# Optimization experiments

Measured on AMD Instinct MI355X. Metric: run time of the kernel, lower is better.

## Reference

```python
import jax, jax.numpy as jnp
import numpy as np

NUM_USERS = 100000
NUM_ITEMS = 50000
D = 64            # args.recdim
N_LAYERS = 3      # args.layer
NNZ = 4800000     # edges in the normalized bipartite adjacency (COO)
N = NUM_USERS + NUM_ITEMS


def setup_inputs() -> dict:
    key = jax.random.key(0)
    k1, k2, k3, k4, k5 = jax.random.split(key, 5)
    # LightGCN inits embeddings with normal(std=0.1)
    user_emb = 0.1 * jax.random.normal(k1, (NUM_USERS, D), dtype=jnp.float32)
    item_emb = 0.1 * jax.random.normal(k2, (NUM_ITEMS, D), dtype=jnp.float32)
    adj_rows = jax.random.randint(k3, (NNZ,), 0, N)
    adj_cols = jax.random.randint(k4, (NNZ,), 0, N)
    # stand-in for D^{-1/2} A D^{-1/2} normalized values
    adj_vals = jax.random.uniform(k5, (NNZ,), dtype=jnp.float32)
    return {"user_emb": user_emb, "item_emb": item_emb,
            "adj_vals": adj_vals, "adj_rows": adj_rows, "adj_cols": adj_cols}


def _spmm(rows, cols, vals, x, n):
    # sparse [n,n] @ dense [n,d] via gather + segment-sum (COO SpMM)
    return jax.ops.segment_sum(vals[:, None] * x[cols], rows, num_segments=n)


def reference(user_emb, item_emb, adj_vals, adj_rows, adj_cols):
    n_users = user_emb.shape[0]
    n = n_users + item_emb.shape[0]
    all_emb = jnp.concatenate([user_emb, item_emb], axis=0)  # [N, D]
    embs = [all_emb]
    for _ in range(N_LAYERS):  # fixed small hop count
        all_emb = _spmm(adj_rows, adj_cols, adj_vals, all_emb, n)
        embs.append(all_emb)
    light_out = jnp.mean(jnp.stack(embs, axis=1), axis=1)  # [N, D]
    users = light_out[:n_users]
    items = light_out[n_users:]
    return users, items
```

## Files before the change

### kernel.cpp

```cpp
#include <hip/hip_runtime.h>


#define NUSERS 100000
#define NITEMS 50000
#define NTOT   150000
#define DIM    64
#define NNZ_E  4800000

#define RPB     256
#define RSH     8
#define NBUCK   586
#define CHUNK_E 16384
#define NPART   ((NNZ_E + CHUNK_E - 1) / CHUNK_E)
#define NBIN    (64 * 37)
#define NOCT    (NBUCK * 64)

__device__ __forceinline__ unsigned short benc(float f) {
    union { float f; unsigned u; } t; t.f = f;
    unsigned r = t.u + 0x7FFFu + ((t.u >> 16) & 1u);
    return (unsigned short)(r >> 16);
}
__device__ __forceinline__ float blo(unsigned g) { return __uint_as_float(g << 16); }
__device__ __forceinline__ float bhi(unsigned g) { return __uint_as_float(g & 0xFFFF0000u); }

__global__ void __launch_bounds__(1024)
partA1_kernel(const int* __restrict__ rows, int* __restrict__ cntmatT) {
    __shared__ int l[NBUCK];
    int p = blockIdx.x;
    int c0 = p * CHUNK_E;
    int c1 = c0 + CHUNK_E; if (c1 > NNZ_E) c1 = NNZ_E;
    for (int k = threadIdx.x; k < NBUCK; k += 1024) l[k] = 0;
    __syncthreads();
    for (int e = c0 + threadIdx.x; e < c1; e += 1024)
        atomicAdd(&l[rows[e] >> RSH], 1);
    __syncthreads();
    for (int k = threadIdx.x; k < NBUCK; k += 1024)
        cntmatT[(size_t)k * NPART + p] = l[k];
}

__global__ void __launch_bounds__(512)
colscan1_kernel(const int* __restrict__ cntmatT, int* __restrict__ runoffT,
                int* __restrict__ colTotal) {
    __shared__ int t[512];
    int b = blockIdx.x;
    int tid = threadIdx.x;
    int v = (tid < NPART) ? cntmatT[(size_t)b * NPART + tid] : 0;
    t[tid] = v;
    __syncthreads();
    for (int ofs = 1; ofs < 512; ofs <<= 1) {
        int a = (tid >= ofs) ? t[tid - ofs] : 0;
        __syncthreads();
        t[tid] += a;
        __syncthreads();
    }
    if (tid < NPART) runoffT[(size_t)b * NPART + tid] = t[tid] - v;
    if (tid == NPART - 1) colTotal[b] = t[tid];
}

__global__ void __launch_bounds__(1024)
colscan2_kernel(const int* __restrict__ colTotal, int* __restrict__ bptr) {
    __shared__ int t[1024];
    int tid = threadIdx.x;
    int v = (tid < NBUCK) ? colTotal[tid] : 0;
    t[tid] = v;
    __syncthreads();
    for (int ofs = 1; ofs < 1024; ofs <<= 1) {
        int a = (tid >= ofs) ? t[tid - ofs] : 0;
        __syncthreads();
        t[tid] += a;
        __syncthreads();
    }
    if (tid < NBUCK) bptr[tid] = t[tid] - v;
    if (tid == 1023) bptr[NBUCK] = t[1023];
}

__global__ void __launch_bounds__(1024)
partA2_kernel(const int* __restrict__ rows, const int* __restrict__ cols,
              const float* __restrict__ vals, const int* __restrict__ runoffT,
              const int* __restrict__ bptr, int2* __restrict__ tmp) {
    __shared__ int cur[NBUCK];
    int p = blockIdx.x;
    int c0 = p * CHUNK_E;
    int c1 = c0 + CHUNK_E; if (c1 > NNZ_E) c1 = NNZ_E;
    for (int k = threadIdx.x; k < NBUCK; k += 1024)
        cur[k] = bptr[k] + runoffT[(size_t)k * NPART + p];
    __syncthreads();
    for (int e = c0 + threadIdx.x; e < c1; e += 1024) {
        int r = rows[e];
        int b = r >> RSH, rl = r & (RPB - 1);
        int q = atomicAdd(&cur[b], 1);
        tmp[q] = make_int2(cols[e] | (rl << 18), __float_as_int(vals[e]));
    }
}

__global__ void __launch_bounds__(1024)
partBF_kernel(const int* __restrict__ bptr, const int2* __restrict__ tmp,
              unsigned* __restrict__ fin, int* __restrict__ optr) {
    __shared__ int cnt[NBIN];
    __shared__ int base[NBIN];
    __shared__ int st[1024];
    int b = blockIdx.x;
    int bb0 = bptr[b];
    int nb = bptr[b + 1] - bb0;
    int tid = threadIdx.x;
    for (int k = tid; k < NBIN; k += 1024) cnt[k] = 0;
    __syncthreads();
    for (int k = tid; k < nb; k += 1024) {
        int x = tmp[bb0 + k].x;
        int key = ((x >> 20) & 63) * 37 + ((x & 0x3FFFF) >> 12);
        atomicAdd(&cnt[key], 1);
    }
    __syncthreads();
    int t0 = tid * 3;
    int c0 = (t0     < NBIN) ? cnt[t0]     : 0;
    int c1 = (t0 + 1 < NBIN) ? cnt[t0 + 1] : 0;
    int c2 = (t0 + 2 < NBIN) ? cnt[t0 + 2] : 0;
    int s = c0 + c1 + c2;
    st[tid] = s;
    __syncthreads();
    for (int ofs = 1; ofs < 1024; ofs <<= 1) {
        int a = (tid >= ofs) ? st[tid - ofs] : 0;
        __syncthreads();
        st[tid] += a;
        __syncthreads();
    }
    int P = st[tid] - s;
    if (t0     < NBIN) base[t0]     = P;
    if (t0 + 1 < NBIN) base[t0 + 1] = P + c0;
    if (t0 + 2 < NBIN) base[t0 + 2] = P + c0 + c1;
    __syncthreads();
    if (tid < 64) optr[b * 64 + tid] = bb0 + base[tid * 37];
    if (b == NBUCK - 1 && tid == 0) optr[NBUCK * 64] = bb0 + nb;
    __syncthreads();
    for (int k = tid; k < nb; k += 1024) {
        int2 t = tmp[bb0 + k];
        int x = t.x;
        int key = ((x >> 20) & 63) * 37 + ((x & 0x3FFFF) >> 12);
        int q = atomicAdd(&base[key], 1);
        unsigned qq = (unsigned)__float2int_rn(__int_as_float(t.y) * 4096.f);
        if (qq > 4095u) qq = 4095u;
        fin[bb0 + q] = ((unsigned)x & 0xFFFFFu) | (qq << 20);
    }
}

__global__ void convert_kernel(const float2* __restrict__ user, const float2* __restrict__ item,
                               unsigned* __restrict__ xh2) {
    int i = blockIdx.x * blockDim.x + threadIdx.x;
    if (i >= NTOT * 32) return;
    float2 v = (i < NUSERS * 32) ? user[i] : item[i - NUSERS * 32];
    xh2[i] = (unsigned)benc(v.x) | ((unsigned)benc(v.y) << 16);
}

__global__ void __launch_bounds__(256)
spmm4_kernel(const int* __restrict__ optr, const unsigned* __restrict__ ed,
             const uint4* __restrict__ xin, uint4* __restrict__ yout,
             const float4* __restrict__ user, const float4* __restrict__ item,
             const uint4* __restrict__ y1, float4* __restrict__ out, int last) {
    int wid  = blockIdx.x * 4 + (threadIdx.x >> 6);
    int lane = threadIdx.x & 63;
    int g    = wid * 8 + (lane >> 3);
    int s    = lane & 7;
    int i    = optr[g];
    int end  = optr[g + 1];
    const float SCL = 1.f / 4096.f;
    float4 A00 = {0,0,0,0}, A01 = {0,0,0,0};
    float4 A10 = {0,0,0,0}, A11 = {0,0,0,0};
    float4 A20 = {0,0,0,0}, A21 = {0,0,0,0};
    float4 A30 = {0,0,0,0}, A31 = {0,0,0,0};

#define PROC(E, G) do { \
        float v  = (float)((E) >> 20) * SCL; \
        int   k  = ((E) >> 18) & 3; \
        float s0 = (k == 0) ? v : 0.f, s1 = (k == 1) ? v : 0.f; \
        float s2 = (k == 2) ? v : 0.f, s3 = (k == 3) ? v : 0.f; \
        float f0 = blo((G).x), f1 = bhi((G).x), f2 = blo((G).y), f3 = bhi((G).y); \
        float f4_ = blo((G).z), f5 = bhi((G).z), f6 = blo((G).w), f7 = bhi((G).w); \
        A00.x += s0*f0; A00.y += s0*f1; A00.z += s0*f2; A00.w += s0*f3; \
        A01.x += s0*f4_; A01.y += s0*f5; A01.z += s0*f6; A01.w += s0*f7; \
        A10.x += s1*f0; A10.y += s1*f1; A10.z += s1*f2; A10.w += s1*f3; \
        A11.x += s1*f4_; A11.y += s1*f5; A11.z += s1*f6; A11.w += s1*f7; \
        A20.x += s2*f0; A20.y += s2*f1; A20.z += s2*f2; A20.w += s2*f3; \
        A21.x += s2*f4_; A21.y += s2*f5; A21.z += s2*f6; A21.w += s2*f7; \
        A30.x += s3*f0; A30.y += s3*f1; A30.z += s3*f2; A30.w += s3*f3; \
        A31.x += s3*f4_; A31.y += s3*f5; A31.z += s3*f6; A31.w += s3*f7; \
    } while (0)

    for (; i + 4 <= end; i += 4) {
        unsigned e0 = ed[i], e1 = ed[i + 1], e2 = ed[i + 2], e3 = ed[i + 3];
        uint4 g0 = xin[(size_t)(e0 & 0x3FFFF) * 8 + s];
        uint4 g1 = xin[(size_t)(e1 & 0x3FFFF) * 8 + s];
        uint4 g2 = xin[(size_t)(e2 & 0x3FFFF) * 8 + s];
        uint4 g3 = xin[(size_t)(e3 & 0x3FFFF) * 8 + s];
        PROC(e0, g0); PROC(e1, g1); PROC(e2, g2); PROC(e3, g3);
    }
    for (; i < end; ++i) {
        unsigned e = ed[i];
        uint4 gg = xin[(size_t)(e & 0x3FFFF) * 8 + s];
        PROC(e, gg);
    }
#undef PROC

    if (!last) {
#define EPI(K, AK0, AK1) do { \
        int r = g * 4 + (K); \
        if (r < NTOT) { \
            uint4 o; \
            o.x = (unsigned)benc(AK0.x) | ((unsigned)benc(AK0.y) << 16); \
            o.y = (unsigned)benc(AK0.z) | ((unsigned)benc(AK0.w) << 16); \
            o.z = (unsigned)benc(AK1.x) | ((unsigned)benc(AK1.y) << 16); \
            o.w = (unsigned)benc(AK1.z) | ((unsigned)benc(AK1.w) << 16); \
            yout[(size_t)r * 8 + s] = o; \
        } \
    } while (0)
        EPI(0, A00, A01); EPI(1, A10, A11); EPI(2, A20, A21); EPI(3, A30, A31);
#undef EPI
    } else {
#define EPI(K, AK0, AK1) do { \
        int r = g * 4 + (K); \
        if (r < NTOT) { \
            size_t f4 = (size_t)r * 16 + 2 * s; \
            float4 x0a = (r < NUSERS) ? user[f4]     : item[f4     - (size_t)NUSERS * 16]; \
            float4 x0b = (r < NUSERS) ? user[f4 + 1] : item[f4 + 1 - (size_t)NUSERS * 16]; \
            uint4 u1 = y1[(size_t)r * 8 + s]; \
            uint4 u2 = xin[(size_t)r * 8 + s]; \
            float4 oa, ob; \
            oa.x = 0.25f * (x0a.x + blo(u1.x) + blo(u2.x) + AK0.x); \
            oa.y = 0.25f * (x0a.y + bhi(u1.x) + bhi(u2.x) + AK0.y); \
            oa.z = 0.25f * (x0a.z + blo(u1.y) + blo(u2.y) + AK0.z); \
            oa.w = 0.25f * (x0a.w + bhi(u1.y) + bhi(u2.y) + AK0.w); \
            ob.x = 0.25f * (x0b.x + blo(u1.z) + blo(u2.z) + AK1.x); \
            ob.y = 0.25f * (x0b.y + bhi(u1.z) + bhi(u2.z) + AK1.y); \
            ob.z = 0.25f * (x0b.z + blo(u1.w) + blo(u2.w) + AK1.z); \
            ob.w = 0.25f * (x0b.w + bhi(u1.w) + bhi(u2.w) + AK1.w); \
            out[f4]     = oa; \
            out[f4 + 1] = ob; \
        } \
    } while (0)
        EPI(0, A00, A01); EPI(1, A10, A11); EPI(2, A20, A21); EPI(3, A30, A31);
#undef EPI
    }
}

extern "C" void kernel_launch(void* const* d_in, const int* in_sizes, int n_in,
                              void* d_out, int out_size, void* d_ws, size_t ws_size,
                              hipStream_t stream) {
    const float* user = (const float*)d_in[0];
    const float* item = (const float*)d_in[1];
    const float* vals = (const float*)d_in[2];
    const int*   rows = (const int*)d_in[3];
    const int*   cols = (const int*)d_in[4];
    float* out = (float*)d_out;

    char* w = (char*)d_ws;
    int2*     tmp      = (int2*)w;     w += (size_t)NNZ_E * 8;
    unsigned* fin      = (unsigned*)w; w += (size_t)NNZ_E * 4;
    unsigned* bufA     = (unsigned*)w; w += (size_t)NTOT * DIM * 2;
    unsigned* bufB     = (unsigned*)w; w += (size_t)NTOT * DIM * 2;
    int*      cntmatT  = (int*)w;      w += (size_t)NBUCK * NPART * 4;
    int*      runoffT  = (int*)w;      w += (size_t)NBUCK * NPART * 4;
    int*      optr     = (int*)w;      w += (size_t)(NOCT + 1) * 4;
    int*      colTotal = (int*)w;      w += (size_t)NBUCK * 4;
    int*      bptr     = (int*)w;

    const int blk = 256;
    const int gConv = (NTOT * 32 + blk - 1) / blk;
    const int gSpmm = NOCT / 32;

    partA1_kernel<<<NPART, 1024, 0, stream>>>(rows, cntmatT);
    colscan1_kernel<<<NBUCK, 512, 0, stream>>>(cntmatT, runoffT, colTotal);
    colscan2_kernel<<<1, 1024, 0, stream>>>(colTotal, bptr);
    partA2_kernel<<<NPART, 1024, 0, stream>>>(rows, cols, vals, runoffT, bptr, tmp);
    partBF_kernel<<<NBUCK, 1024, 0, stream>>>(bptr, tmp, fin, optr);

    convert_kernel<<<gConv, blk, 0, stream>>>((const float2*)user, (const float2*)item, bufA);

    spmm4_kernel<<<gSpmm, blk, 0, stream>>>(optr, fin, (const uint4*)bufA, (uint4*)bufB,
                                            (const float4*)user, (const float4*)item,
                                            (const uint4*)bufB, (float4*)out, 0);
    spmm4_kernel<<<gSpmm, blk, 0, stream>>>(optr, fin, (const uint4*)bufB, (uint4*)bufA,
                                            (const float4*)user, (const float4*)item,
                                            (const uint4*)bufB, (float4*)out, 0);
    spmm4_kernel<<<gSpmm, blk, 0, stream>>>(optr, fin, (const uint4*)bufA, (uint4*)bufA,
                                            (const float4*)user, (const float4*)item,
                                            (const uint4*)bufB, (float4*)out, 1);
}
```

Baseline: 492.2 us.

## Sort edges locally in shared memory per chunk and gather segments in bucket pass

The first partition pass now sorts each chunk's edges by bucket in LDS and writes the chunk out contiguously, instead of scattering each edge straight to its global bucket position. The bucket pass then locates each bucket's segments across chunks with a binary search over per-chunk offsets. The chunk size is halved to fit the LDS buffer, and the fine-bin count is doubled with a smaller column shift, which changes the edge ordering inside each octet. The aim is to replace scattered global writes with coalesced ones, at the cost of scattered-segment reads and a binary search per edge in the bucket pass.

```diff
diff --git a/kernel.cpp b/kernel.cpp
--- a/kernel.cpp
+++ b/kernel.cpp
@@ -10,9 +10,11 @@
 #define RPB     256
 #define RSH     8
 #define NBUCK   586
-#define CHUNK_E 16384
+#define CHUNK_E 8192
 #define NPART   ((NNZ_E + CHUNK_E - 1) / CHUNK_E)
-#define NBIN    (64 * 37)
+#define NCB     74
+#define CSH     11
+#define NBIN    (64 * NCB)
 #define NOCT    (NBUCK * 64)
 
 __device__ __forceinline__ unsigned short benc(float f) {
@@ -23,38 +25,41 @@
 __device__ __forceinline__ float blo(unsigned g) { return __uint_as_float(g << 16); }
 __device__ __forceinline__ float bhi(unsigned g) { return __uint_as_float(g & 0xFFFF0000u); }
 
-__global__ void __launch_bounds__(1024)
-partA1_kernel(const int* __restrict__ rows, int* __restrict__ cntmatT) {
+__global__ void __launch_bounds__(512)
+partA1_kernel(const int* __restrict__ rows, int* __restrict__ cntmat) {
     __shared__ int l[NBUCK];
     int p = blockIdx.x;
     int c0 = p * CHUNK_E;
     int c1 = c0 + CHUNK_E; if (c1 > NNZ_E) c1 = NNZ_E;
-    for (int k = threadIdx.x; k < NBUCK; k += 1024) l[k] = 0;
-    __syncthreads();
-    for (int e = c0 + threadIdx.x; e < c1; e += 1024)
+    for (int k = threadIdx.x; k < NBUCK; k += 512) l[k] = 0;
+    __syncthreads();
+    for (int e = c0 + threadIdx.x; e < c1; e += 512)
         atomicAdd(&l[rows[e] >> RSH], 1);
     __syncthreads();
-    for (int k = threadIdx.x; k < NBUCK; k += 1024)
-        cntmatT[(size_t)k * NPART + p] = l[k];
-}
-
-__global__ void __launch_bounds__(512)
-colscan1_kernel(const int* __restrict__ cntmatT, int* __restrict__ runoffT,
+    for (int k = threadIdx.x; k < NBUCK; k += 512)
+        cntmat[(size_t)p * NBUCK + k] = l[k];
+}
+
+__global__ void __launch_bounds__(1024)
+colscan1_kernel(const int* __restrict__ cntmat, int* __restrict__ runoffT,
                 int* __restrict__ colTotal) {
-    __shared__ int t[512];
+    __shared__ int t[1024];
     int b = blockIdx.x;
     int tid = threadIdx.x;
-    int v = (tid < NPART) ? cntmatT[(size_t)b * NPART + tid] : 0;
+    int v = (tid < NPART) ? cntmat[(size_t)tid * NBUCK + b] : 0;
     t[tid] = v;
     __syncthreads();
-    for (int ofs = 1; ofs < 512; ofs <<= 1) {
+    for (int ofs = 1; ofs < 1024; ofs <<= 1) {
         int a = (tid >= ofs) ? t[tid - ofs] : 0;
         __syncthreads();
         t[tid] += a;
         __syncthreads();
     }
-    if (tid < NPART) runoffT[(size_t)b * NPART + tid] = t[tid] - v;
-    if (tid == NPART - 1) colTotal[b] = t[tid];
+    if (tid < NPART) runoffT[(size_t)b * (NPART + 1) + tid] = t[tid] - v;
+    if (tid == NPART - 1) {
+        runoffT[(size_t)b * (NPART + 1) + NPART] = t[tid];
+        colTotal[b] = t[tid];
+    }
 }
 
 __global__ void __launch_bounds__(1024)
@@ -74,48 +79,78 @@
     if (tid == 1023) bptr[NBUCK] = t[1023];
 }
 
-__global__ void __launch_bounds__(1024)
+__global__ void __launch_bounds__(512)
 partA2_kernel(const int* __restrict__ rows, const int* __restrict__ cols,
-              const float* __restrict__ vals, const int* __restrict__ runoffT,
-              const int* __restrict__ bptr, int2* __restrict__ tmp) {
+              const float* __restrict__ vals, const int* __restrict__ cntmat,
+              int* __restrict__ segoff, int2* __restrict__ tmp) {
+    __shared__ int2 buf[CHUNK_E];
     __shared__ int cur[NBUCK];
+    __shared__ int st[512];
     int p = blockIdx.x;
     int c0 = p * CHUNK_E;
     int c1 = c0 + CHUNK_E; if (c1 > NNZ_E) c1 = NNZ_E;
-    for (int k = threadIdx.x; k < NBUCK; k += 1024)
-        cur[k] = bptr[k] + runoffT[(size_t)k * NPART + p];
-    __syncthreads();
-    for (int e = c0 + threadIdx.x; e < c1; e += 1024) {
+    int nb = c1 - c0;
+    int tid = threadIdx.x;
+    int t0 = tid * 2;
+    int cA = (t0     < NBUCK) ? cntmat[(size_t)p * NBUCK + t0]     : 0;
+    int cB = (t0 + 1 < NBUCK) ? cntmat[(size_t)p * NBUCK + t0 + 1] : 0;
+    int s = cA + cB;
+    st[tid] = s;
+    __syncthreads();
+    for (int ofs = 1; ofs < 512; ofs <<= 1) {
+        int a = (tid >= ofs) ? st[tid - ofs] : 0;
+        __syncthreads();
+        st[tid] += a;
+        __syncthreads();
+    }
+    int P = st[tid] - s;
+    if (t0     < NBUCK) { cur[t0]     = P;      segoff[(size_t)p * NBUCK + t0]     = P; }
+    if (t0 + 1 < NBUCK) { cur[t0 + 1] = P + cA; segoff[(size_t)p * NBUCK + t0 + 1] = P + cA; }
+    __syncthreads();
+    for (int e = c0 + tid; e < c1; e += 512) {
         int r = rows[e];
         int b = r >> RSH, rl = r & (RPB - 1);
         int q = atomicAdd(&cur[b], 1);
-        tmp[q] = make_int2(cols[e] | (rl << 18), __float_as_int(vals[e]));
-    }
+        buf[q] = make_int2(cols[e] | (rl << 18), __float_as_int(vals[e]));
+    }
+    __syncthreads();
+    for (int k = tid; k < nb; k += 512)
+        tmp[c0 + k] = buf[k];
 }
 
 __global__ void __launch_bounds__(1024)
-partBF_kernel(const int* __restrict__ bptr, const int2* __restrict__ tmp,
+partBF_kernel(const int* __restrict__ bptr, const int* __restrict__ runoffT,
+              const int* __restrict__ segoff, const int2* __restrict__ tmp,
               unsigned* __restrict__ fin, int* __restrict__ optr) {
     __shared__ int cnt[NBIN];
     __shared__ int base[NBIN];
     __shared__ int st[1024];
+    __shared__ int runoff[NPART + 1];
+    __shared__ int soff[NPART];
     int b = blockIdx.x;
     int bb0 = bptr[b];
-    int nb = bptr[b + 1] - bb0;
     int tid = threadIdx.x;
     for (int k = tid; k < NBIN; k += 1024) cnt[k] = 0;
-    __syncthreads();
-    for (int k = tid; k < nb; k += 1024) {
-        int x = tmp[bb0 + k].x;
-        int key = ((x >> 20) & 63) * 37 + ((x & 0x3FFFF) >> 12);
+    if (tid <= NPART) runoff[tid] = runoffT[(size_t)b * (NPART + 1) + tid];
+    if (tid < NPART)  soff[tid]   = segoff[(size_t)tid * NBUCK + b];
+    __syncthreads();
+    int nb = runoff[NPART];
+    for (int j = tid; j < nb; j += 1024) {
+        int lo = 0, hi = NPART;
+        while (hi - lo > 1) { int mid = (lo + hi) >> 1; if (runoff[mid] <= j) lo = mid; else hi = mid; }
+        int src = lo * CHUNK_E + soff[lo] + (j - runoff[lo]);
+        int x = tmp[src].x;
+        int key = ((x >> 20) & 63) * NCB + ((x & 0x3FFFF) >> CSH);
         atomicAdd(&cnt[key], 1);
     }
     __syncthreads();
-    int t0 = tid * 3;
+    int t0 = tid * 5;
     int c0 = (t0     < NBIN) ? cnt[t0]     : 0;
     int c1 = (t0 + 1 < NBIN) ? cnt[t0 + 1] : 0;
     int c2 = (t0 + 2 < NBIN) ? cnt[t0 + 2] : 0;
-    int s = c0 + c1 + c2;
+    int c3 = (t0 + 3 < NBIN) ? cnt[t0 + 3] : 0;
+    int c4 = (t0 + 4 < NBIN) ? cnt[t0 + 4] : 0;
+    int s = c0 + c1 + c2 + c3 + c4;
     st[tid] = s;
     __syncthreads();
     for (int ofs = 1; ofs < 1024; ofs <<= 1) {
@@ -128,14 +163,19 @@
     if (t0     < NBIN) base[t0]     = P;
     if (t0 + 1 < NBIN) base[t0 + 1] = P + c0;
     if (t0 + 2 < NBIN) base[t0 + 2] = P + c0 + c1;
-    __syncthreads();
-    if (tid < 64) optr[b * 64 + tid] = bb0 + base[tid * 37];
+    if (t0 + 3 < NBIN) base[t0 + 3] = P + c0 + c1 + c2;
+    if (t0 + 4 < NBIN) base[t0 + 4] = P + c0 + c1 + c2 + c3;
+    __syncthreads();
+    if (tid < 64) optr[b * 64 + tid] = bb0 + base[tid * NCB];
     if (b == NBUCK - 1 && tid == 0) optr[NBUCK * 64] = bb0 + nb;
     __syncthreads();
-    for (int k = tid; k < nb; k += 1024) {
-        int2 t = tmp[bb0 + k];
+    for (int j = tid; j < nb; j += 1024) {
+        int lo = 0, hi = NPART;
+        while (hi - lo > 1) { int mid = (lo + hi) >> 1; if (runoff[mid] <= j) lo = mid; else hi = mid; }
+        int src = lo * CHUNK_E + soff[lo] + (j - runoff[lo]);
+        int2 t = tmp[src];
         int x = t.x;
-        int key = ((x >> 20) & 63) * 37 + ((x & 0x3FFFF) >> 12);
+        int key = ((x >> 20) & 63) * NCB + ((x & 0x3FFFF) >> CSH);
         int q = atomicAdd(&base[key], 1);
         unsigned qq = (unsigned)__float2int_rn(__int_as_float(t.y) * 4096.f);
         if (qq > 4095u) qq = 4095u;
@@ -256,8 +296,9 @@
     unsigned* fin      = (unsigned*)w; w += (size_t)NNZ_E * 4;
     unsigned* bufA     = (unsigned*)w; w += (size_t)NTOT * DIM * 2;
     unsigned* bufB     = (unsigned*)w; w += (size_t)NTOT * DIM * 2;
-    int*      cntmatT  = (int*)w;      w += (size_t)NBUCK * NPART * 4;
-    int*      runoffT  = (int*)w;      w += (size_t)NBUCK * NPART * 4;
+    int*      cntmat   = (int*)w;      w += (size_t)NPART * NBUCK * 4;
+    int*      runoffT  = (int*)w;      w += (size_t)NBUCK * (NPART + 1) * 4;
+    int*      segoff   = (int*)w;      w += (size_t)NPART * NBUCK * 4;
     int*      optr     = (int*)w;      w += (size_t)(NOCT + 1) * 4;
     int*      colTotal = (int*)w;      w += (size_t)NBUCK * 4;
     int*      bptr     = (int*)w;
@@ -266,11 +307,11 @@
     const int gConv = (NTOT * 32 + blk - 1) / blk;
     const int gSpmm = NOCT / 32;
 
-    partA1_kernel<<<NPART, 1024, 0, stream>>>(rows, cntmatT);
-    colscan1_kernel<<<NBUCK, 512, 0, stream>>>(cntmatT, runoffT, colTotal);
+    partA1_kernel<<<NPART, 512, 0, stream>>>(rows, cntmat);
+    colscan1_kernel<<<NBUCK, 1024, 0, stream>>>(cntmat, runoffT, colTotal);
     colscan2_kernel<<<1, 1024, 0, stream>>>(colTotal, bptr);
-    partA2_kernel<<<NPART, 1024, 0, stream>>>(rows, cols, vals, runoffT, bptr, tmp);
-    partBF_kernel<<<NBUCK, 1024, 0, stream>>>(bptr, tmp, fin, optr);
+    partA2_kernel<<<NPART, 512, 0, stream>>>(rows, cols, vals, cntmat, segoff, tmp);
+    partBF_kernel<<<NBUCK, 1024, 0, stream>>>(bptr, runoffT, segoff, tmp, fin, optr);
 
     convert_kernel<<<gConv, blk, 0, stream>>>((const float2*)user, (const float2*)item, bufA);
 
```

Measured after the change: 475.0 us. 3.5% less time.
